# Optimization experiments

Hardware: AMD Instinct MI355X
Metric: run time of the kernel (lower is better)

## Reference

```python
import jax, jax.numpy as jnp
import numpy as np

BN_EPS = 1e-5


def setup_inputs() -> dict:
    key = jax.random.key(0)
    ks = jax.random.split(key, 6)
    B, D, C, H, S = 2, 48, 16, 128, 8
    x = jax.random.normal(ks[0], (B, D, D, D, C), dtype=jnp.float32)
    # depthwise Conv3d(channel_n, channel_n, k=7, groups=channel_n): DHWIO kernel, I=1
    conv_w = jax.random.normal(ks[1], (7, 7, 7, 1, C), dtype=jnp.float32) * 0.05
    conv_b = jnp.zeros((C,), jnp.float32)
    fc0_w = jax.random.normal(ks[2], (2 * C, H), dtype=jnp.float32) * (1.0 / np.sqrt(2.0 * C))
    fc0_b = jnp.zeros((H,), jnp.float32)
    # torch zero-inits fc1; randomized small so the baseline computes nontrivial math
    fc1_w = jax.random.normal(ks[3], (H, C), dtype=jnp.float32) * 0.02
    bn_gamma = jnp.ones((H,), jnp.float32)
    bn_beta = jnp.zeros((H,), jnp.float32)
    # stochastic fire mask: torch.rand > 0.5  ==  Bernoulli(0.5)  ==  randint(0,2)
    masks = jax.random.randint(ks[4], (S, B, D, D, D, 1), 0, 2, dtype=jnp.int32)
    return {"x": x, "conv_w": conv_w, "conv_b": conv_b, "fc0_w": fc0_w,
            "fc0_b": fc0_b, "fc1_w": fc1_w, "bn_gamma": bn_gamma,
            "bn_beta": bn_beta, "masks": masks, "steps": 8, "input_channels": 1}


def _update(x, conv_w, conv_b, fc0_w, fc0_b, fc1_w, bn_gamma, bn_beta, mask):
    # x: [B, X, Y, Z, C] channels-last
    C = x.shape[-1]
    p = (conv_w.shape[0] - 1) // 2
    xp = jnp.pad(x, ((0, 0), (p, p), (p, p), (p, p), (0, 0)), mode="reflect")
    y1 = jax.lax.conv_general_dilated(
        xp, conv_w, window_strides=(1, 1, 1), padding="VALID",
        dimension_numbers=("NDHWC", "DHWIO", "NDHWC"),
        feature_group_count=C) + conv_b
    y = jnp.concatenate([x, y1], axis=-1)            # perceive: [B,X,Y,Z,2C]
    h = y @ fc0_w + fc0_b                            # [B,X,Y,Z,H]
    # BatchNorm3d(track_running_stats=False): batch stats over (B, spatial)
    mean = jnp.mean(h, axis=(0, 1, 2, 3))
    var = jnp.var(h, axis=(0, 1, 2, 3))              # biased variance
    h = (h - mean) * jax.lax.rsqrt(var + BN_EPS) * bn_gamma + bn_beta
    h = jax.nn.relu(h)
    dx = (h @ fc1_w) * mask.astype(x.dtype)          # stochastic fire, then residual
    return x + dx


def reference(x, conv_w, conv_b, fc0_w, fc0_b, fc1_w, bn_gamma, bn_beta, masks, steps, input_channels):
    for i in range(steps):
        x2 = _update(x, conv_w, conv_b, fc0_w, fc0_b, fc1_w, bn_gamma, bn_beta, masks[i])
        # input channels stay frozen; state channels evolve
        x = jnp.concatenate([x[..., :input_channels], x2[..., input_channels:]], axis=-1)
    return x
```

## Files before the change

kernel.cpp:

```cpp
#include <hip/hip_runtime.h>

#define D 48
#define C 16
#define H 128
#define D3 (D*D*D)
#define NVOX (2*D3)
#define NB_FC (NVOX/128)
#define BN_EPS 1e-5f

#define PROW 56
#define PPL  (54*PROW)
#define PVOL (54*PPL)
#define NPAD (54*54*54)

typedef unsigned short u16;
typedef unsigned int   u32;
typedef __attribute__((ext_vector_type(8))) short bf16x8;
typedef __attribute__((ext_vector_type(4))) float f32x4;

__device__ __forceinline__ float bf2f(u16 u) {
    union { u32 i; float f; } p; p.i = ((u32)u) << 16; return p.f;
}
__device__ __forceinline__ float lof(u32 u) {
    union { u32 i; float f; } p; p.i = u << 16; return p.f;
}
__device__ __forceinline__ float hif(u32 u) {
    union { u32 i; float f; } p; p.i = u & 0xFFFF0000u; return p.f;
}
__device__ __forceinline__ u16 f2bf(float f) {
    union { float f; u32 i; } p; p.f = f;
    u32 r = p.i + 0x7fffu + ((p.i >> 16) & 1u);
    return (u16)(r >> 16);
}
__device__ __forceinline__ int refl(int i) {
    return i < 0 ? -i : (i >= D ? 2*D - 2 - i : i);
}

__global__ __launch_bounds__(256)
void k_pad0(const float* __restrict__ x, u16* __restrict__ xp) {
    const int idx = blockIdx.x * 256 + threadIdx.x;
    const int bc = idx / NPAD;
    int r = idx - bc * NPAD;
    const int pz = r / 2916; r -= pz * 2916;
    const int py = r / 54;
    const int px = r - py * 54;
    const int b = bc >> 4, c = bc & 15;
    const int z = refl(pz - 3), y = refl(py - 3), x0 = refl(px - 3);
    xp[(size_t)bc*PVOL + pz*PPL + py*PROW + px] =
        f2bf(x[(((size_t)(b*D + z))*D + y)*D*C + x0*C + c]);
}

__global__ __launch_bounds__(256)
void k_halo(u16* __restrict__ xp) {
    const int idx = blockIdx.x * 256 + threadIdx.x;
    const int bc = idx / NPAD;
    int r = idx - bc * NPAD;
    const int pz = r / 2916; r -= pz * 2916;
    const int py = r / 54;
    const int px = r - py * 54;
    if (pz >= 3 && pz < 51 && py >= 3 && py < 51 && px >= 3 && px < 51) return;
    const int sz = refl(pz-3) + 3, sy = refl(py-3) + 3, sx = refl(px-3) + 3;
    xp[(size_t)bc*PVOL + pz*PPL + py*PROW + px] =
        xp[(size_t)bc*PVOL + sz*PPL + sy*PROW + sx];
}

__global__ __launch_bounds__(256)
void k_wxpose(const float* __restrict__ cw, float* __restrict__ wt,
              const float* __restrict__ w0, uint4* __restrict__ w0f,
              const float* __restrict__ w1, uint4* __restrict__ w1f) {
    int i = blockIdx.x * 256 + threadIdx.x;
    if (i < 343 * 16) {
        int kidx = i >> 4, c = i & 15;
        int dz = kidx / 49, dy = (kidx / 7) % 7, dx = kidx % 7;
        wt[((c*7 + dy)*7 + dz)*7 + dx] = cw[i];
    }
    if (i < 512) {
        const int jt = i >> 6, l = i & 63;
        const int j = jt*16 + (l & 15), k0 = (l >> 4) * 8;
        u32 v[8];
        #pragma unroll
        for (int q = 0; q < 8; ++q) v[q] = f2bf(w0[(size_t)(k0+q)*H + j]);
        uint4 o = { v[0] | (v[1]<<16), v[2] | (v[3]<<16),
                    v[4] | (v[5]<<16), v[6] | (v[7]<<16) };
        w0f[jt*64 + l] = o;
    }
    if (i < 256) {
        const int kk = i >> 6, l = i & 63;
        const int col = l & 15, k0 = kk*32 + (l >> 4) * 8;
        u32 v[8];
        #pragma unroll
        for (int q = 0; q < 8; ++q) v[q] = f2bf(w1[(size_t)(k0+q)*C + col]);
        uint4 o = { v[0] | (v[1]<<16), v[2] | (v[3]<<16),
                    v[4] | (v[5]<<16), v[6] | (v[7]<<16) };
        w1f[kk*64 + l] = o;
    }
}

__global__ __launch_bounds__(192)
void k_conv(const u16* __restrict__ xp, const float* __restrict__ wt,
            const float* __restrict__ cbias, u16* __restrict__ y1m) {
    const int bid = blockIdx.x;
    const int zt = bid & 15;
    const int yt = (bid >> 4) % 3;
    const int c  = (bid / 48) & 15;
    const int b  = bid / 768;
    const int t  = threadIdx.x;
    const int tx = t % 12, ty = t / 12;
    const int y0 = yt * 16, z0 = zt * 3;
    const u16* base = xp + (size_t)(b*16 + c) * PVOL
                         + (size_t)(y0 + ty) * PROW + 4*tx
                         + (size_t)z0 * PPL;
    const float* wc = wt + c * 343;

    float a[3][4];
    #pragma unroll
    for (int k = 0; k < 3; ++k)
        a[k][0] = a[k][1] = a[k][2] = a[k][3] = 0.f;

    for (int dy = 0; dy < 7; ++dy) {
        float w[49];
        const float* wrow = wc + dy*49;
        #pragma unroll
        for (int q = 0; q < 12; ++q) {
            float4 p = *(const float4*)(wrow + q*4);
            w[q*4+0] = p.x; w[q*4+1] = p.y; w[q*4+2] = p.z; w[q*4+3] = p.w;
        }
        w[48] = wrow[48];
        const u16* rowb = base + (size_t)dy * PROW;
        #pragma unroll
        for (int pz = 0; pz < 9; ++pz) {
            const u16* rp = rowb + (size_t)pz * PPL;
            const uint2 p01 = *(const uint2*)rp;
            const uint2 p23 = *(const uint2*)(rp + 4);
            const u32  p4  = *(const u32*)(rp + 8);
            const float v0 = lof(p01.x), v1 = hif(p01.x);
            const float v2 = lof(p01.y), v3 = hif(p01.y);
            const float v4 = lof(p23.x), v5 = hif(p23.x);
            const float v6 = lof(p23.y), v7 = hif(p23.y);
            const float v8 = lof(p4),    v9 = hif(p4);
            #pragma unroll
            for (int k = 0; k < 3; ++k) {
                const int dz = pz - k;
                if (dz >= 0 && dz <= 6) {
                    const float w0=w[dz*7+0], w1=w[dz*7+1], w2=w[dz*7+2],
                                w3=w[dz*7+3], w4=w[dz*7+4], w5=w[dz*7+5],
                                w6=w[dz*7+6];
                    a[k][0] = fmaf(w0,v0, fmaf(w1,v1, fmaf(w2,v2, fmaf(w3,v3,
                              fmaf(w4,v4, fmaf(w5,v5, fmaf(w6,v6, a[k][0])))))));
                    a[k][1] = fmaf(w0,v1, fmaf(w1,v2, fmaf(w2,v3, fmaf(w3,v4,
                              fmaf(w4,v5, fmaf(w5,v6, fmaf(w6,v7, a[k][1])))))));
                    a[k][2] = fmaf(w0,v2, fmaf(w1,v3, fmaf(w2,v4, fmaf(w3,v5,
                              fmaf(w4,v6, fmaf(w5,v7, fmaf(w6,v8, a[k][2])))))));
                    a[k][3] = fmaf(w0,v3, fmaf(w1,v4, fmaf(w2,v5, fmaf(w3,v6,
                              fmaf(w4,v7, fmaf(w5,v8, fmaf(w6,v9, a[k][3])))))));
                }
            }
        }
    }

    const float cbv = cbias[c];
    const size_t cb_off = (size_t)(b*16 + c) * D3;
    #pragma unroll
    for (int k = 0; k < 3; ++k) {
        const size_t sp = (size_t)(z0+k)*2304 + (y0+ty)*48 + 4*tx;
        ushort4 o = { f2bf(a[k][0]+cbv), f2bf(a[k][1]+cbv),
                      f2bf(a[k][2]+cbv), f2bf(a[k][3]+cbv) };
        *(ushort4*)(y1m + cb_off + sp) = o;
    }
}

__device__ __forceinline__ bf16x8 fc0_afrag(const float* __restrict__ srcx,
                                            const u16 (*ys)[128],
                                            int vb0, int vfeed, int ks) {
    bf16x8 A;
    if (ks < 2) {
        const float4* xp4 = (const float4*)(srcx + (size_t)(vb0+vfeed)*C + ks*8);
        float4 p0 = xp4[0], p1 = xp4[1];
        A[0]=(short)f2bf(p0.x); A[1]=(short)f2bf(p0.y);
        A[2]=(short)f2bf(p0.z); A[3]=(short)f2bf(p0.w);
        A[4]=(short)f2bf(p1.x); A[5]=(short)f2bf(p1.y);
        A[6]=(short)f2bf(p1.z); A[7]=(short)f2bf(p1.w);
    } else {
        const int c0 = (ks - 2) * 8;
        #pragma unroll
        for (int i = 0; i < 8; ++i) A[i] = (short)ys[c0+i][vfeed];
    }
    return A;
}

__global__ __launch_bounds__(256)
void k_fc0(const float* __restrict__ srcx, const u16* __restrict__ y1m,
           const uint4* __restrict__ w0f, const float* __restrict__ b0,
           float* __restrict__ partials) {
    __shared__ u16 ys[16][128];
    __shared__ float red[2][128][17];
    const int t = threadIdx.x;
    const int lane = t & 63, wv = t >> 6;
    const int vb0 = blockIdx.x * 128;
    const int b  = vb0 / D3;
    const int sp0 = vb0 - b * D3;
    {
        const u16* yb = y1m + (size_t)b*16*D3 + sp0;
        #pragma unroll
        for (int r = 0; r < 2; ++r) {
            const int idx = t + 256*r;
            const int cc = idx >> 5, q = idx & 31;
            *(ushort4*)&ys[cc][q*4] = *(const ushort4*)(yb + (size_t)cc*D3 + q*4);
        }
    }
    uint4 Bf[8];
    #pragma unroll
    for (int jt = 0; jt < 8; ++jt) Bf[jt] = w0f[jt*64 + lane];
    float bias[8];
    #pragma unroll
    for (int jt = 0; jt < 8; ++jt) bias[jt] = b0[jt*16 + (lane & 15)];
    __syncthreads();

    float sumr[8], sqr[8];
    #pragma unroll
    for (int jt = 0; jt < 8; ++jt) { sumr[jt] = 0.f; sqr[jt] = 0.f; }

    const int vx = lane & 15, ks = lane >> 4;
    #pragma unroll
    for (int tile = 0; tile < 2; ++tile) {
        const int vfeed = wv*32 + tile*16 + vx;
        bf16x8 A = fc0_afrag(srcx, ys, vb0, vfeed, ks);
        #pragma unroll
        for (int jt = 0; jt < 8; ++jt) {
            f32x4 acc = { bias[jt], bias[jt], bias[jt], bias[jt] };
            acc = __builtin_amdgcn_mfma_f32_16x16x32_bf16(
                      A, *(bf16x8*)&Bf[jt], acc, 0, 0, 0);
            #pragma unroll
            for (int r = 0; r < 4; ++r) {
                const float h = acc[r];
                sumr[jt] += h; sqr[jt] = fmaf(h, h, sqr[jt]);
            }
        }
    }
    #pragma unroll
    for (int jt = 0; jt < 8; ++jt) {
        red[0][jt*16 + vx][wv*4 + ks] = sumr[jt];
        red[1][jt*16 + vx][wv*4 + ks] = sqr[jt];
    }
    __syncthreads();
    const int stat = t >> 7, j = t & 127;
    float acc = 0.f;
    #pragma unroll
    for (int g = 0; g < 16; ++g) acc += red[stat][j][g];
    partials[(size_t)t * NB_FC + blockIdx.x] = acc;
}

__global__ __launch_bounds__(256)
void k_red(const float* __restrict__ partials, float* __restrict__ sums) {
    const int s = blockIdx.x, t = threadIdx.x;
    const float* row = partials + (size_t)s * NB_FC;
    float a = 0.f;
    for (int i = t; i < NB_FC; i += 256) a += row[i];
    __shared__ float l[256];
    l[t] = a; __syncthreads();
    if (t < 128) l[t] += l[t + 128];
    __syncthreads();
    if (t < 64) {
        float v = l[t] + l[t + 64];
        #pragma unroll
        for (int off = 32; off; off >>= 1) v += __shfl_down(v, off);
        if (t == 0) sums[s] = v;
    }
}

__global__ __launch_bounds__(256)
void k_apply(const float* __restrict__ srcx, const u16* __restrict__ y1m,
             const uint4* __restrict__ w0f, const float* __restrict__ b0,
             const uint4* __restrict__ w1f,
             const float* __restrict__ gamma, const float* __restrict__ beta,
             const float* __restrict__ sums, const int* __restrict__ mask,
             float* __restrict__ xo, u16* __restrict__ xp) {
    __shared__ u16 ys[16][128];
    __shared__ u16 hp[128][132];
    __shared__ float xs[16][132];
    const int t = threadIdx.x;
    const int lane = t & 63, wv = t >> 6;
    const int vb0 = blockIdx.x * 128;
    const int b  = vb0 / D3;
    const int sp0 = vb0 - b * D3;
    {
        const u16* yb = y1m + (size_t)b*16*D3 + sp0;
        #pragma unroll
        for (int r = 0; r < 2; ++r) {
            const int idx = t + 256*r;
            const int cc = idx >> 5, q = idx & 31;
            *(ushort4*)&ys[cc][q*4] = *(const ushort4*)(yb + (size_t)cc*D3 + q*4);
        }
    }
    const int vx = lane & 15, ks = lane >> 4;
    uint4 Bf[8];
    #pragma unroll
    for (int jt = 0; jt < 8; ++jt) Bf[jt] = w0f[jt*64 + lane];
    float bias[8];
    #pragma unroll
    for (int jt = 0; jt < 8; ++jt) bias[jt] = b0[jt*16 + vx];
    uint4 W1f[4];
    #pragma unroll
    for (int kk = 0; kk < 4; ++kk) W1f[kk] = w1f[kk*64 + lane];
    float scv[8], shv[8];
    {
        const float invN = 1.0f / (float)NVOX;
        #pragma unroll
        for (int jt = 0; jt < 8; ++jt) {
            const int jj = jt*16 + vx;
            const float mean = sums[jj] * invN;
            const float var  = fmaf(-mean, mean, sums[H + jj] * invN);
            const float rr = rsqrtf(var + BN_EPS);
            scv[jt] = gamma[jj] * rr;
            shv[jt] = beta[jj] - mean * scv[jt];
        }
    }
    __syncthreads();

    #pragma unroll
    for (int tile = 0; tile < 2; ++tile) {
        const int vfeed = wv*32 + tile*16 + vx;
        bf16x8 A = fc0_afrag(srcx, ys, vb0, vfeed, ks);
        const int vrow0 = wv*32 + tile*16 + (ks << 2);
        #pragma unroll
        for (int jt = 0; jt < 8; ++jt) {
            f32x4 acc = { bias[jt], bias[jt], bias[jt], bias[jt] };
            acc = __builtin_amdgcn_mfma_f32_16x16x32_bf16(
                      A, *(bf16x8*)&Bf[jt], acc, 0, 0, 0);
            const int jj = jt*16 + vx;
            #pragma unroll
            for (int r = 0; r < 4; ++r) {
                const float hq = fmaxf(0.f, fmaf(acc[r], scv[jt], shv[jt]));
                hp[vrow0 + r][jj] = f2bf(hq);
            }
        }
    }
    #pragma unroll
    for (int tile = 0; tile < 2; ++tile) {
        const int vfeed = wv*32 + tile*16 + vx;
        f32x4 acc1 = { 0.f, 0.f, 0.f, 0.f };
        #pragma unroll
        for (int kk = 0; kk < 4; ++kk) {
            union { uint4 u; bf16x8 v; } a1;
            const uint2 q0 = *(const uint2*)&hp[vfeed][kk*32 + ks*8];
            const uint2 q1 = *(const uint2*)&hp[vfeed][kk*32 + ks*8 + 4];
            a1.u.x = q0.x; a1.u.y = q0.y; a1.u.z = q1.x; a1.u.w = q1.y;
            acc1 = __builtin_amdgcn_mfma_f32_16x16x32_bf16(
                       a1.v, *(bf16x8*)&W1f[kk], acc1, 0, 0, 0);
        }
        const int vrow0 = wv*32 + tile*16 + (ks << 2);
        #pragma unroll
        for (int r = 0; r < 4; ++r) {
            const int vl = vrow0 + r;
            const size_t v = (size_t)vb0 + vl;
            const float m = (float)mask[v];
            const float xold = srcx[v*C + vx];
            const float xn = (vx == 0) ? xold : fmaf(acc1[r], m, xold);
            xo[v*C + vx] = xn;
            xs[vx][vl] = xn;
        }
    }
    __syncthreads();
    #pragma unroll
    for (int r = 0; r < 8; ++r) {
        const int idx = t + 256*r;
        const int c2 = idx >> 7, vi = idx & 127;
        const int s = sp0 + vi;
        const int z = s / 2304, rem = s - z*2304;
        const int yy = rem / 48, x0 = rem - yy*48;
        xp[(size_t)(b*16 + c2)*PVOL + (size_t)(z+3)*PPL
           + (yy+3)*PROW + (x0+3)] = f2bf(xs[c2][vi]);
    }
}

extern "C" void kernel_launch(void* const* d_in, const int* in_sizes, int n_in,
                              void* d_out, int out_size, void* d_ws, size_t ws_size,
                              hipStream_t stream) {
    const float* x_in = (const float*)d_in[0];
    const float* cw   = (const float*)d_in[1];
    const float* cb   = (const float*)d_in[2];
    const float* w0   = (const float*)d_in[3];
    const float* b0   = (const float*)d_in[4];
    const float* w1   = (const float*)d_in[5];
    const float* gm   = (const float*)d_in[6];
    const float* bt   = (const float*)d_in[7];
    const int*   mk   = (const int*)d_in[8];
    float* out = (float*)d_out;

    char* p = (char*)d_ws;
    u16*   xp       = (u16*)p;     p += (size_t)32 * PVOL * 2;
    u16*   y1m      = (u16*)p;     p += (size_t)NVOX * C * 2;
    float* partials = (float*)p;   p += (size_t)256 * NB_FC * 4;
    float* sums     = (float*)p;   p += 256 * 4;
    float* wt       = (float*)p;   p += 343 * 16 * 4;
    uint4* w0f      = (uint4*)p;   p += 512 * 16;
    uint4* w1f      = (uint4*)p;   p += 256 * 16;

    k_pad0  <<<32*NPAD/256, 256, 0, stream>>>(x_in, xp);
    k_wxpose<<<22,          256, 0, stream>>>(cw, wt, w0, w0f, w1, w1f);
    for (int s = 0; s < 8; ++s) {
        const float* srcx = (s == 0) ? x_in : out;
        k_conv <<<1536,  192, 0, stream>>>(xp, wt, cb, y1m);
        k_fc0  <<<NB_FC, 256, 0, stream>>>(srcx, y1m, w0f, b0, partials);
        k_red  <<<256,   256, 0, stream>>>(partials, sums);
        k_apply<<<NB_FC, 256, 0, stream>>>(srcx, y1m, w0f, b0, w1f, gm, bt,
                                           sums, mk + (size_t)s * NVOX, out, xp);
        if (s < 7) k_halo<<<32*NPAD/256, 256, 0, stream>>>(xp);
    }
}
```

Before: 699.8 us.

## Store padded conv input as fp16 and use packed fdot2 in depthwise conv

Switches the padded state buffer and the conv weights from bf16/fp32 to fp16 and rewrites the 7x7x7 depthwise conv inner loop to use v_dot2 (fdot2) on packed half pairs, with alignbit providing the odd-shifted pairs. This halves the number of multiply-accumulate instructions and removes the per-element bf16-to-fp32 unpacking. Weights are repacked into dx-pair u32 words, with a zero pad for the eighth tap. It trades bf16's range for fp16 precision on the state, which carries overflow risk if the state grows large.

```diff
diff --git a/kernel.cpp b/kernel.cpp
--- a/kernel.cpp
+++ b/kernel.cpp
@@ -1,4 +1,5 @@
 #include <hip/hip_runtime.h>
+#include <hip/hip_fp16.h>
 
 #define D 48
 #define C 16
@@ -17,20 +18,21 @@
 typedef unsigned int   u32;
 typedef __attribute__((ext_vector_type(8))) short bf16x8;
 typedef __attribute__((ext_vector_type(4))) float f32x4;
+typedef __attribute__((ext_vector_type(2))) _Float16 h16x2;
 
 __device__ __forceinline__ float bf2f(u16 u) {
     union { u32 i; float f; } p; p.i = ((u32)u) << 16; return p.f;
-}
-__device__ __forceinline__ float lof(u32 u) {
-    union { u32 i; float f; } p; p.i = u << 16; return p.f;
-}
-__device__ __forceinline__ float hif(u32 u) {
-    union { u32 i; float f; } p; p.i = u & 0xFFFF0000u; return p.f;
 }
 __device__ __forceinline__ u16 f2bf(float f) {
     union { float f; u32 i; } p; p.f = f;
     u32 r = p.i + 0x7fffu + ((p.i >> 16) & 1u);
     return (u16)(r >> 16);
+}
+__device__ __forceinline__ u16 f2h(float f) {
+    return __half_as_ushort(__float2half(f));
+}
+__device__ __forceinline__ h16x2 ash2(u32 u) {
+    union { u32 i; h16x2 h; } p; p.i = u; return p.h;
 }
 __device__ __forceinline__ int refl(int i) {
     return i < 0 ? -i : (i >= D ? 2*D - 2 - i : i);
@@ -47,7 +49,7 @@
     const int b = bc >> 4, c = bc & 15;
     const int z = refl(pz - 3), y = refl(py - 3), x0 = refl(px - 3);
     xp[(size_t)bc*PVOL + pz*PPL + py*PROW + px] =
-        f2bf(x[(((size_t)(b*D + z))*D + y)*D*C + x0*C + c]);
+        f2h(x[(((size_t)(b*D + z))*D + y)*D*C + x0*C + c]);
 }
 
 __global__ __launch_bounds__(256)
@@ -65,14 +67,20 @@
 }
 
 __global__ __launch_bounds__(256)
-void k_wxpose(const float* __restrict__ cw, float* __restrict__ wt,
+void k_wxpose(const float* __restrict__ cw, u32* __restrict__ wt2,
               const float* __restrict__ w0, uint4* __restrict__ w0f,
               const float* __restrict__ w1, uint4* __restrict__ w1f) {
     int i = blockIdx.x * 256 + threadIdx.x;
-    if (i < 343 * 16) {
-        int kidx = i >> 4, c = i & 15;
-        int dz = kidx / 49, dy = (kidx / 7) % 7, dx = kidx % 7;
-        wt[((c*7 + dy)*7 + dz)*7 + dx] = cw[i];
+    if (i < 784) {
+        const int c = i / 49, r = i % 49;
+        const int dy = r / 7, dz = r % 7;
+        #pragma unroll
+        for (int q = 0; q < 4; ++q) {
+            const int dx0 = 2*q, dx1 = 2*q + 1;
+            u32 h0 = f2h(cw[((dz*7 + dy)*7 + dx0)*C + c]);
+            u32 h1 = (dx1 < 7) ? f2h(cw[((dz*7 + dy)*7 + dx1)*C + c]) : 0u;
+            wt2[(size_t)i*4 + q] = h0 | (h1 << 16);
+        }
     }
     if (i < 512) {
         const int jt = i >> 6, l = i & 63;
@@ -97,7 +105,7 @@
 }
 
 __global__ __launch_bounds__(192)
-void k_conv(const u16* __restrict__ xp, const float* __restrict__ wt,
+void k_conv(const u16* __restrict__ xp, const u32* __restrict__ wt2,
             const float* __restrict__ cbias, u16* __restrict__ y1m) {
     const int bid = blockIdx.x;
     const int zt = bid & 15;
@@ -110,7 +118,6 @@
     const u16* base = xp + (size_t)(b*16 + c) * PVOL
                          + (size_t)(y0 + ty) * PROW + 4*tx
                          + (size_t)z0 * PPL;
-    const float* wc = wt + c * 343;
 
     float a[3][4];
     #pragma unroll
@@ -118,14 +125,13 @@
         a[k][0] = a[k][1] = a[k][2] = a[k][3] = 0.f;
 
     for (int dy = 0; dy < 7; ++dy) {
-        float w[49];
-        const float* wrow = wc + dy*49;
-        #pragma unroll
-        for (int q = 0; q < 12; ++q) {
-            float4 p = *(const float4*)(wrow + q*4);
-            w[q*4+0] = p.x; w[q*4+1] = p.y; w[q*4+2] = p.z; w[q*4+3] = p.w;
-        }
-        w[48] = wrow[48];
+        u32 W[7][4];
+        const u32* wr = wt2 + ((size_t)(c*7 + dy)*7)*4;
+        #pragma unroll
+        for (int dz = 0; dz < 7; ++dz) {
+            W[dz][0] = wr[dz*4+0]; W[dz][1] = wr[dz*4+1];
+            W[dz][2] = wr[dz*4+2]; W[dz][3] = wr[dz*4+3];
+        }
         const u16* rowb = base + (size_t)dy * PROW;
         #pragma unroll
         for (int pz = 0; pz < 9; ++pz) {
@@ -133,26 +139,25 @@
             const uint2 p01 = *(const uint2*)rp;
             const uint2 p23 = *(const uint2*)(rp + 4);
             const u32  p4  = *(const u32*)(rp + 8);
-            const float v0 = lof(p01.x), v1 = hif(p01.x);
-            const float v2 = lof(p01.y), v3 = hif(p01.y);
-            const float v4 = lof(p23.x), v5 = hif(p23.x);
-            const float v6 = lof(p23.y), v7 = hif(p23.y);
-            const float v8 = lof(p4),    v9 = hif(p4);
+            u32 P[5] = { p01.x, p01.y, p23.x, p23.y, p4 };
+            u32 Q[5];
+            #pragma unroll
+            for (int i = 0; i < 4; ++i)
+                Q[i] = __builtin_amdgcn_alignbit(P[i+1], P[i], 16);
+            Q[4] = P[4] >> 16;
             #pragma unroll
             for (int k = 0; k < 3; ++k) {
                 const int dz = pz - k;
                 if (dz >= 0 && dz <= 6) {
-                    const float w0=w[dz*7+0], w1=w[dz*7+1], w2=w[dz*7+2],
-                                w3=w[dz*7+3], w4=w[dz*7+4], w5=w[dz*7+5],
-                                w6=w[dz*7+6];
-                    a[k][0] = fmaf(w0,v0, fmaf(w1,v1, fmaf(w2,v2, fmaf(w3,v3,
-                              fmaf(w4,v4, fmaf(w5,v5, fmaf(w6,v6, a[k][0])))))));
-                    a[k][1] = fmaf(w0,v1, fmaf(w1,v2, fmaf(w2,v3, fmaf(w3,v4,
-                              fmaf(w4,v5, fmaf(w5,v6, fmaf(w6,v7, a[k][1])))))));
-                    a[k][2] = fmaf(w0,v2, fmaf(w1,v3, fmaf(w2,v4, fmaf(w3,v5,
-                              fmaf(w4,v6, fmaf(w5,v7, fmaf(w6,v8, a[k][2])))))));
-                    a[k][3] = fmaf(w0,v3, fmaf(w1,v4, fmaf(w2,v5, fmaf(w3,v6,
-                              fmaf(w4,v7, fmaf(w5,v8, fmaf(w6,v9, a[k][3])))))));
+                    const u32* Wz = W[dz];
+                    #pragma unroll
+                    for (int q = 0; q < 4; ++q) {
+                        const h16x2 wq = ash2(Wz[q]);
+                        a[k][0] = __builtin_amdgcn_fdot2(ash2(P[q]),   wq, a[k][0], false);
+                        a[k][1] = __builtin_amdgcn_fdot2(ash2(Q[q]),   wq, a[k][1], false);
+                        a[k][2] = __builtin_amdgcn_fdot2(ash2(P[q+1]), wq, a[k][2], false);
+                        a[k][3] = __builtin_amdgcn_fdot2(ash2(Q[q+1]), wq, a[k][3], false);
+                    }
                 }
             }
         }
@@ -369,7 +374,7 @@
         const int z = s / 2304, rem = s - z*2304;
         const int yy = rem / 48, x0 = rem - yy*48;
         xp[(size_t)(b*16 + c2)*PVOL + (size_t)(z+3)*PPL
-           + (yy+3)*PROW + (x0+3)] = f2bf(xs[c2][vi]);
+           + (yy+3)*PROW + (x0+3)] = f2h(xs[c2][vi]);
     }
 }
 
@@ -392,15 +397,15 @@
     u16*   y1m      = (u16*)p;     p += (size_t)NVOX * C * 2;
     float* partials = (float*)p;   p += (size_t)256 * NB_FC * 4;
     float* sums     = (float*)p;   p += 256 * 4;
-    float* wt       = (float*)p;   p += 343 * 16 * 4;
+    u32*   wt2      = (u32*)p;     p += 784 * 4 * 4;
     uint4* w0f      = (uint4*)p;   p += 512 * 16;
     uint4* w1f      = (uint4*)p;   p += 256 * 16;
 
     k_pad0  <<<32*NPAD/256, 256, 0, stream>>>(x_in, xp);
-    k_wxpose<<<22,          256, 0, stream>>>(cw, wt, w0, w0f, w1, w1f);
+    k_wxpose<<<22,          256, 0, stream>>>(cw, wt2, w0, w0f, w1, w1f);
     for (int s = 0; s < 8; ++s) {
         const float* srcx = (s == 0) ? x_in : out;
-        k_conv <<<1536,  192, 0, stream>>>(xp, wt, cb, y1m);
+        k_conv <<<1536,  192, 0, stream>>>(xp, wt2, cb, y1m);
         k_fc0  <<<NB_FC, 256, 0, stream>>>(srcx, y1m, w0f, b0, partials);
         k_red  <<<256,   256, 0, stream>>>(partials, sums);
         k_apply<<<NB_FC, 256, 0, stream>>>(srcx, y1m, w0f, b0, w1f, gm, bt,
```

Result: faster. 632.6 us (-9.6%).
